# Kernel tuning notes

Hardware: AMD Instinct MI355X
Metric: run time of the kernel (lower is better)

Reference implementation:

```python
import jax, jax.numpy as jnp
import numpy as np

B, H, W = 16, 128, 128
D = 64          # embedding_dim
K = 1024        # num_embeddings
CC = 0.25       # commitment_cost
KLD = 10.0      # kld_scale


def setup_inputs() -> dict:
    key = jax.random.key(0)
    k1, k2, k3, k4, k5, k6 = jax.random.split(key, 6)
    # xavier-uniform-ish codebook init
    lim = float(np.sqrt(6.0 / (K + D)))
    return {
        "x": jax.random.normal(k1, (B, 1, H, W), dtype=jnp.float32),
        "w_in": jax.random.normal(k2, (D,), dtype=jnp.float32),   # Conv2d(1,D,1) weight
        "b_in": jax.random.normal(k3, (D,), dtype=jnp.float32) * 0.1,
        "emb": jax.random.uniform(k4, (K, D), dtype=jnp.float32, minval=-lim, maxval=lim),
        "w_out": jax.random.normal(k5, (D,), dtype=jnp.float32),  # Conv2d(D,1,1) weight
        "b_out": jax.random.normal(k6, (1,), dtype=jnp.float32) * 0.1,
    }


def reference(x, w_in, b_in, emb, w_out, b_out):
    sg = jax.lax.stop_gradient
    # in_proj: 1x1 conv with 1 input channel == per-pixel scale+bias, NCHW -> NHWC-D
    h = x[:, 0, :, :, None] * w_in + b_in               # [B,H,W,D]
    flat = h.reshape(-1, D)                             # [N,D]
    # squared L2 distances to codebook: ||f||^2 - 2 f.e + ||e||^2
    dist = (jnp.sum(flat * flat, axis=1, keepdims=True)
            - 2.0 * flat @ emb.T
            + jnp.sum(emb * emb, axis=1))               # [N,K]
    idx = jnp.argmin(dist, axis=1).reshape(B, H, W)     # nearest code
    q = emb[idx]                                        # [B,H,W,D] gather
    emb_loss = KLD * (CC * jnp.mean((sg(q) - h) ** 2)
                      + jnp.mean((q - sg(h)) ** 2))
    q_st = h + sg(q - h)                                # straight-through
    # out_proj: 1x1 conv D->1
    out = (jnp.einsum("bhwd,d->bhw", q_st, w_out) + b_out[0])[:, None]  # [B,1,H,W]
    return out, emb_loss
```

## Files before the change

### kernel.cpp

```cpp
#include <hip/hip_runtime.h>


#define VQ_K 1024
#define VQ_D 64
#define NPIX 262144

__global__ __launch_bounds__(256) void k_prep(const float* __restrict__ emb,
                                              const float* __restrict__ w_in,
                                              const float* __restrict__ b_in,
                                              const float* __restrict__ w_out,
                                              double* __restrict__ ws) {
    int lane = threadIdx.x & 63;
    int k = blockIdx.x * 4 + (threadIdx.x >> 6);
    double w  = (double)w_in[lane];
    double b  = (double)b_in[lane];
    double wo = (double)w_out[lane];
    double e  = (double)emb[k * VQ_D + lane];

    double p = e * w, r = e * b, c = e * e, t = e * wo;
    for (int off = 32; off > 0; off >>= 1) {
        p += __shfl_xor(p, off, 64);
        r += __shfl_xor(r, off, 64);
        c += __shfl_xor(c, off, 64);
        t += __shfl_xor(t, off, 64);
    }
    if (lane == 0) {
        ws[k]        = c - 2.0 * r;
        ws[1024 + k] = -2.0 * p;
        ws[2048 + k] = t;
    }
    if (k == 0) {
        double W2 = w * w, WB = w * b, B2 = b * b;
        for (int off = 32; off > 0; off >>= 1) {
            W2 += __shfl_xor(W2, off, 64);
            WB += __shfl_xor(WB, off, 64);
            B2 += __shfl_xor(B2, off, 64);
        }
        if (lane == 0) {
            ws[6144] = W2; ws[6145] = WB; ws[6146] = B2;
            ((int*)(ws + 6148))[0] = 0;
        }
    }
}

__global__ __launch_bounds__(256) void k_env(double* __restrict__ ws) {
    const double* A = ws;
    const double* M = ws + 1024;
    int lane = threadIdx.x & 63;
    int k = blockIdx.x * 4 + (threadIdx.x >> 6);
    double ak = A[k], mk = M[k];
    double lo = -1e300, hi = 1e300;
    int dom = 0;
    #pragma unroll 4
    for (int t = 0; t < 16; ++t) {
        int j = lane + (t << 6);
        if (j == k) continue;
        double aj = A[j], mj = M[j];
        if (mj == mk) {
            if (aj < ak || (aj == ak && j < k)) dom = 1;
        } else {
            double xx = (aj - ak) / (mk - mj);
            if (mj > mk) lo = fmax(lo, xx);
            else         hi = fmin(hi, xx);
        }
    }
    for (int off = 32; off > 0; off >>= 1) {
        lo   = fmax(lo, __shfl_xor(lo, off, 64));
        hi   = fmin(hi, __shfl_xor(hi, off, 64));
        dom |= __shfl_xor(dom, off, 64);
    }
    if (lane == 0 && !dom && lo < hi) {
        int s = atomicAdd((int*)(ws + 6148), 1);
        ws[3072 + s] = ak;
        ws[4096 + s] = mk;
        ws[5120 + s] = ws[2048 + k];
    }
}

__global__ __launch_bounds__(256) void k_pix(const float* __restrict__ x,
                                             const float* __restrict__ b_out,
                                             double* __restrict__ ws,
                                             float* __restrict__ out) {
    __shared__ double sA[VQ_K], sM[VQ_K], sT[VQ_K];
    __shared__ double red[4];
    int S = ((const int*)(ws + 6148))[0];
    for (int i = threadIdx.x; i < S; i += 256) {
        sA[i] = ws[3072 + i];
        sM[i] = ws[4096 + i];
        sT[i] = ws[5120 + i];
    }
    double W2 = ws[6144], WB = ws[6145], B2 = ws[6146];
    double bo = (double)b_out[0];
    __syncthreads();

    int gid = blockIdx.x * 256 + threadIdx.x;
    float4 xv4 = ((const float4*)x)[gid];
    double xv[4] = {(double)xv4.x, (double)xv4.y, (double)xv4.z, (double)xv4.w};
    double best[4] = {1e300, 1e300, 1e300, 1e300};
    double bt[4]   = {0.0, 0.0, 0.0, 0.0};

    for (int s = 0; s < S; ++s) {
        double a = sA[s], m = sM[s], t = sT[s];
        #pragma unroll
        for (int p = 0; p < 4; ++p) {
            double v = fma(xv[p], m, a);
            if (v < best[p]) { best[p] = v; bt[p] = t; }
        }
    }

    float4 o;
    o.x = (float)(bt[0] + bo);
    o.y = (float)(bt[1] + bo);
    o.z = (float)(bt[2] + bo);
    o.w = (float)(bt[3] + bo);
    ((float4*)out)[gid] = o;

    double s = 0.0;
    #pragma unroll
    for (int p = 0; p < 4; ++p)
        s += best[p] + xv[p] * xv[p] * W2 + 2.0 * xv[p] * WB + B2;

    for (int off = 32; off > 0; off >>= 1) s += __shfl_down(s, off, 64);
    int lane = threadIdx.x & 63, wid = threadIdx.x >> 6;
    if (lane == 0) red[wid] = s;
    __syncthreads();
    if (threadIdx.x == 0) {
        double bs = red[0] + red[1] + red[2] + red[3];
        atomicAdd(&out[NPIX], (float)(bs * (12.5 / 16777216.0)));
    }
}

extern "C" void kernel_launch(void* const* d_in, const int* in_sizes, int n_in,
                              void* d_out, int out_size, void* d_ws, size_t ws_size,
                              hipStream_t stream) {
    const float* x     = (const float*)d_in[0];
    const float* w_in  = (const float*)d_in[1];
    const float* b_in  = (const float*)d_in[2];
    const float* emb   = (const float*)d_in[3];
    const float* w_out = (const float*)d_in[4];
    const float* b_out = (const float*)d_in[5];
    float* out = (float*)d_out;
    double* ws = (double*)d_ws;

    hipLaunchKernelGGL(k_prep, dim3(256),       dim3(256), 0, stream, emb, w_in, b_in, w_out, ws);
    hipLaunchKernelGGL(k_env,  dim3(256),       dim3(256), 0, stream, ws);
    hipLaunchKernelGGL(k_pix,  dim3(NPIX/1024), dim3(256), 0, stream, x, b_out, ws, out);
}
```

Baseline: 79.76 us.

## Fuse codebook prep into envelope kernel and compact codes per block

Merges the prep and envelope kernels into one launch. Every block redundantly recomputes all 1024 codebook line coefficients into shared memory, so the separate launch and the global round trip between them go away. The global atomic counter is replaced by fixed per-code slots, with invalid codes marked by a sentinel. Each pixel block then compacts the valid codes into shared memory using a shared atomic. This trades one kernel launch for redundant per-block work, and it makes the order of surviving codes nondeterministic, which can affect tie handling.

Result: slower. 86.19 us (+8.1%).

```diff
diff --git a/kernel.cpp b/kernel.cpp
--- a/kernel.cpp
+++ b/kernel.cpp
@@ -5,57 +5,75 @@
 #define VQ_D 64
 #define NPIX 262144
 
-__global__ __launch_bounds__(256) void k_prep(const float* __restrict__ emb,
+__global__ __launch_bounds__(256) void vq_env(const float* __restrict__ emb,
                                               const float* __restrict__ w_in,
                                               const float* __restrict__ b_in,
                                               const float* __restrict__ w_out,
                                               double* __restrict__ ws) {
-    int lane = threadIdx.x & 63;
-    int k = blockIdx.x * 4 + (threadIdx.x >> 6);
-    double w  = (double)w_in[lane];
-    double b  = (double)b_in[lane];
-    double wo = (double)w_out[lane];
-    double e  = (double)emb[k * VQ_D + lane];
+    __shared__ double sA[VQ_K], sM[VQ_K];
+    __shared__ double swd[VQ_D], sbd[VQ_D];
+    int tid = threadIdx.x;
+    if (tid < 64) { swd[tid] = (double)w_in[tid]; sbd[tid] = (double)b_in[tid]; }
+    __syncthreads();
 
-    double p = e * w, r = e * b, c = e * e, t = e * wo;
-    for (int off = 32; off > 0; off >>= 1) {
-        p += __shfl_xor(p, off, 64);
-        r += __shfl_xor(r, off, 64);
-        c += __shfl_xor(c, off, 64);
-        t += __shfl_xor(t, off, 64);
+    int lane = tid & 63;
+    int wv   = tid >> 6;
+    int grp  = lane >> 2;
+    int sub  = lane & 3;
+
+    for (int pass = 0; pass < 16; ++pass) {
+        int line = wv * 256 + pass * 16 + grp;
+        const float4* e4 = (const float4*)(emb + line * VQ_D + sub * 16);
+        double p = 0.0, r = 0.0, cc = 0.0;
+        #pragma unroll
+        for (int q = 0; q < 4; ++q) {
+            float4 v = e4[q];
+            int d0 = sub * 16 + q * 4;
+            double e0 = (double)v.x, e1 = (double)v.y;
+            double e2 = (double)v.z, e3 = (double)v.w;
+            p  = fma(e0, swd[d0],     p);
+            p  = fma(e1, swd[d0 + 1], p);
+            p  = fma(e2, swd[d0 + 2], p);
+            p  = fma(e3, swd[d0 + 3], p);
+            r  = fma(e0, sbd[d0],     r);
+            r  = fma(e1, sbd[d0 + 1], r);
+            r  = fma(e2, sbd[d0 + 2], r);
+            r  = fma(e3, sbd[d0 + 3], r);
+            cc = fma(e0, e0, cc);
+            cc = fma(e1, e1, cc);
+            cc = fma(e2, e2, cc);
+            cc = fma(e3, e3, cc);
+        }
+        p  += __shfl_xor(p, 1, 64);  p  += __shfl_xor(p, 2, 64);
+        r  += __shfl_xor(r, 1, 64);  r  += __shfl_xor(r, 2, 64);
+        cc += __shfl_xor(cc, 1, 64); cc += __shfl_xor(cc, 2, 64);
+        if (sub == 0) {
+            sA[line] = cc - 2.0 * r;
+            sM[line] = -2.0 * p;
+        }
     }
-    if (lane == 0) {
-        ws[k]        = c - 2.0 * r;
-        ws[1024 + k] = -2.0 * p;
-        ws[2048 + k] = t;
-    }
-    if (k == 0) {
+    __syncthreads();
+
+    if (blockIdx.x == 0 && tid < 64) {
+        double w = swd[tid], b = sbd[tid];
         double W2 = w * w, WB = w * b, B2 = b * b;
         for (int off = 32; off > 0; off >>= 1) {
             W2 += __shfl_xor(W2, off, 64);
             WB += __shfl_xor(WB, off, 64);
             B2 += __shfl_xor(B2, off, 64);
         }
-        if (lane == 0) {
-            ws[6144] = W2; ws[6145] = WB; ws[6146] = B2;
-            ((int*)(ws + 6148))[0] = 0;
-        }
+        if (tid == 0) { ws[6144] = W2; ws[6145] = WB; ws[6146] = B2; }
     }
-}
 
-__global__ __launch_bounds__(256) void k_env(double* __restrict__ ws) {
-    const double* A = ws;
-    const double* M = ws + 1024;
-    int lane = threadIdx.x & 63;
-    int k = blockIdx.x * 4 + (threadIdx.x >> 6);
-    double ak = A[k], mk = M[k];
+    int k = blockIdx.x * 4 + wv;
+    double ak = sA[k], mk = sM[k];
     double lo = -1e300, hi = 1e300;
     int dom = 0;
     #pragma unroll 4
     for (int t = 0; t < 16; ++t) {
         int j = lane + (t << 6);
         if (j == k) continue;
-        double aj = A[j], mj = M[j];
+        double aj = sA[j], mj = sM[j];
         if (mj == mk) {
             if (aj < ak || (aj == ak && j < k)) dom = 1;
         } else {
@@ -64,36 +82,46 @@
             else         hi = fmin(hi, xx);
         }
     }
+    double tval = (double)emb[k * VQ_D + lane] * (double)w_out[lane];
     for (int off = 32; off > 0; off >>= 1) {
         lo   = fmax(lo, __shfl_xor(lo, off, 64));
         hi   = fmin(hi, __shfl_xor(hi, off, 64));
         dom |= __shfl_xor(dom, off, 64);
+        tval += __shfl_xor(tval, off, 64);
     }
-    if (lane == 0 && !dom && lo < hi) {
-        int s = atomicAdd((int*)(ws + 6148), 1);
-        ws[3072 + s] = ak;
-        ws[4096 + s] = mk;
-        ws[5120 + s] = ws[2048 + k];
+    if (lane == 0) {
+        bool valid = (!dom) && (lo < hi);
+        ws[3072 + k] = valid ? ak : 1e300;
+        ws[4096 + k] = valid ? mk : 0.0;
+        ws[5120 + k] = tval;
     }
 }
 
-__global__ __launch_bounds__(256) void k_pix(const float* __restrict__ x,
-                                             const float* __restrict__ b_out,
-                                             double* __restrict__ ws,
-                                             float* __restrict__ out) {
+__global__ __launch_bounds__(256) void vq_pix(const float* __restrict__ x,
+                                              const float* __restrict__ b_out,
+                                              const double* __restrict__ ws,
+                                              float* __restrict__ out) {
     __shared__ double sA[VQ_K], sM[VQ_K], sT[VQ_K];
     __shared__ double red[4];
-    int S = ((const int*)(ws + 6148))[0];
-    for (int i = threadIdx.x; i < S; i += 256) {
-        sA[i] = ws[3072 + i];
-        sM[i] = ws[4096 + i];
-        sT[i] = ws[5120 + i];
+    __shared__ int scnt;
+    int tid = threadIdx.x;
+    if (tid == 0) scnt = 0;
+    __syncthreads();
+    for (int i = tid; i < VQ_K; i += 256) {
+        double a = ws[3072 + i];
+        if (a < 1e299) {
+            int s = atomicAdd(&scnt, 1);
+            sA[s] = a;
+            sM[s] = ws[4096 + i];
+            sT[s] = ws[5120 + i];
+        }
     }
     double W2 = ws[6144], WB = ws[6145], B2 = ws[6146];
     double bo = (double)b_out[0];
     __syncthreads();
+    int S = scnt;
 
-    int gid = blockIdx.x * 256 + threadIdx.x;
+    int gid = blockIdx.x * 256 + tid;
     float4 xv4 = ((const float4*)x)[gid];
     double xv[4] = {(double)xv4.x, (double)xv4.y, (double)xv4.z, (double)xv4.w};
     double best[4] = {1e300, 1e300, 1e300, 1e300};
@@ -121,10 +149,10 @@
         s += best[p] + xv[p] * xv[p] * W2 + 2.0 * xv[p] * WB + B2;
 
     for (int off = 32; off > 0; off >>= 1) s += __shfl_down(s, off, 64);
-    int lane = threadIdx.x & 63, wid = threadIdx.x >> 6;
+    int lane = tid & 63, wid = tid >> 6;
     if (lane == 0) red[wid] = s;
     __syncthreads();
-    if (threadIdx.x == 0) {
+    if (tid == 0) {
         double bs = red[0] + red[1] + red[2] + red[3];
         atomicAdd(&out[NPIX], (float)(bs * (12.5 / 16777216.0)));
     }
@@ -142,7 +170,8 @@
     float* out = (float*)d_out;
     double* ws = (double*)d_ws;
 
-    hipLaunchKernelGGL(k_prep, dim3(256),       dim3(256), 0, stream, emb, w_in, b_in, w_out, ws);
-    hipLaunchKernelGGL(k_env,  dim3(256),       dim3(256), 0, stream, ws);
-    hipLaunchKernelGGL(k_pix,  dim3(NPIX/1024), dim3(256), 0, stream, x, b_out, ws, out);
+    hipLaunchKernelGGL(vq_env, dim3(256),       dim3(256), 0, stream,
+                       emb, w_in, b_in, w_out, ws);
+    hipLaunchKernelGGL(vq_pix, dim3(NPIX/1024), dim3(256), 0, stream,
+                       x, b_out, ws, out);
 }
```
